# Kernel tuning notes

Hardware: AMD Instinct MI355X
Metric: run time of the kernel (lower is better)

## Reference

```python
import jax, jax.numpy as jnp
import numpy as np

B, T, D, U = 64, 2048, 256, 256
EPS = 1e-6


def setup_inputs() -> dict:
    key = jax.random.key(0)
    ks = jax.random.split(key, 4)
    x = jax.random.normal(ks[0], (B, T, D), dtype=jnp.float32)
    # glorot-ish scaled init for stability
    kernel = jax.random.normal(ks[1], (D, 3 * U), dtype=jnp.float32) * (1.0 / np.sqrt(D))
    rec_kernel = jax.random.normal(ks[2], (U, 3 * U), dtype=jnp.float32) * (1.0 / np.sqrt(U))
    bias = jnp.zeros((3 * U,), dtype=jnp.float32)
    ln_gamma = jnp.ones((U,), dtype=jnp.float32)
    ln_beta = jnp.zeros((U,), dtype=jnp.float32)
    return {"x": x, "kernel": kernel, "rec_kernel": rec_kernel, "bias": bias,
            "ln_gamma": ln_gamma, "ln_beta": ln_beta}


def _custom_gru(x, kernel, rec_kernel, bias):
    # Precompute input projection for all timesteps: [B,T,3U]
    xw = jnp.einsum('btd,dk->btk', x, kernel) + bias
    xw_t = jnp.swapaxes(xw, 0, 1)  # [T,B,3U] for scan
    h0 = jnp.zeros((x.shape[0], U), dtype=x.dtype)

    def step(h, xw_step):
        gates = xw_step + h @ rec_kernel            # [B,3U]
        z, r, h_hat_pre = jnp.split(gates, 3, axis=1)
        z = jax.nn.sigmoid(z)
        r = jax.nn.sigmoid(r)
        # nonstandard blend inside tanh (faithful to CustomGRUCell)
        h_hat = jnp.tanh(r * h_hat_pre + (1.0 - r) * h)
        h_new = (1.0 - z) * h_hat + z * h
        return h_new, h_new

    _, hs = jax.lax.scan(step, h0, xw_t)            # hs: [T,B,U]
    return jnp.swapaxes(hs, 0, 1)                   # [B,T,U]


def _layernorm(x, gamma, beta):
    mu = jnp.mean(x, axis=-1, keepdims=True)
    var = jnp.mean(jnp.square(x - mu), axis=-1, keepdims=True)
    return (x - mu) * jax.lax.rsqrt(var + EPS) * gamma + beta


def reference(x, kernel, rec_kernel, bias, ln_gamma, ln_beta):
    # call() returns only the GRU-stack branch (n=1 layer) + shared LayerNorm;
    # the embedded_inputs branch in the source is dead code.
    seq = _custom_gru(x, kernel, rec_kernel, bias)
    return _layernorm(seq, ln_gamma, ln_beta)
```

## Files before the change

### kernel.cpp

```cpp
#include <hip/hip_runtime.h>
#include <hip/hip_bf16.h>
#include <hip/hip_fp16.h>

using half2_t = __attribute__((ext_vector_type(2))) _Float16;
using half8_t = __attribute__((ext_vector_type(8))) _Float16;
using f32x4   = __attribute__((ext_vector_type(4))) float;
using i32x4   = __attribute__((ext_vector_type(4))) int;

#define B_   64
#define T_   2048
#define D_   256
#define U_   256
#define NG   768
#define TC   512
#define NCHUNK (T_/TC)
#define GB_SCAN 16
#define GB_GEMM 1536
#define GB_LN   2048

typedef const __attribute__((address_space(1))) void* gptr_t;
typedef __attribute__((address_space(3))) void* lptr_t;

__device__ __forceinline__ float rcpf(float x) { return __builtin_amdgcn_rcpf(x); }


__global__ void conv_x_chunk(const float* __restrict__ x, _Float16* __restrict__ xh, int t0) {
  size_t idx = ((size_t)blockIdx.x * 256 + threadIdx.x) * 8;
  int b   = (int)(idx >> 17);
  int rem = (int)(idx & 131071);
  const float4* p = (const float4*)(x + ((size_t)(b * T_ + t0)) * D_ + rem);
  float4 v0 = p[0], v1 = p[1];
  half8_t o;
  o[0] = (_Float16)v0.x; o[1] = (_Float16)v0.y; o[2] = (_Float16)v0.z; o[3] = (_Float16)v0.w;
  o[4] = (_Float16)v1.x; o[5] = (_Float16)v1.y; o[6] = (_Float16)v1.z; o[7] = (_Float16)v1.w;
  *(half8_t*)(xh + idx) = o;
}

__global__ void conv_T(const float* __restrict__ src, _Float16* __restrict__ dst) {
  int idx = blockIdx.x * 256 + threadIdx.x;
  int d = idx / NG;
  int j = idx - d * NG;
  dst[j * 256 + d] = (_Float16)src[idx];
}

__global__ void init_scale(unsigned* s) { if (threadIdx.x == 0) *s = 0u; }

__global__ void absmax_rec(const float* __restrict__ rec, unsigned* __restrict__ s) {
  int i = (blockIdx.x * 256 + threadIdx.x) * 4;
  float4 v = *(const float4*)(rec + i);
  float m = fmaxf(fmaxf(fabsf(v.x), fabsf(v.y)), fmaxf(fabsf(v.z), fabsf(v.w)));
  #pragma unroll
  for (int off = 32; off >= 1; off >>= 1) m = fmaxf(m, __shfl_xor(m, off));
  __shared__ float sm[4];
  int l = threadIdx.x & 63, wv = threadIdx.x >> 6;
  if (l == 0) sm[wv] = m;
  __syncthreads();
  if (threadIdx.x == 0) {
    m = fmaxf(fmaxf(sm[0], sm[1]), fmaxf(sm[2], sm[3]));
    atomicMax(s, __float_as_uint(m));
  }
}

__global__ void conv_rec_i8(const float* __restrict__ rec, const unsigned* __restrict__ sc,
                            char* __restrict__ dst) {
  int idx = blockIdx.x * 256 + threadIdx.x;
  int j = idx & 15, l = (idx >> 4) & 63, sl = idx >> 10;
  int mt = sl >> 2, ks = sl & 3, bi = l & 15, hi = l >> 4;
  float am = __uint_as_float(*sc) + 1e-30f;
  float s = 127.f / am;
  float v = rec[(size_t)(ks * 64 + hi * 16 + j) * NG + mt * 16 + bi] * s;
  int q = __float2int_rn(v);
  q = q > 127 ? 127 : (q < -127 ? -127 : q);
  dst[idx] = (char)q;
}


__global__ __launch_bounds__(1024) void mega(
    const char* __restrict__ rq,
    const _Float16* __restrict__ xwsS,
    const unsigned* __restrict__ sc,
    float* __restrict__ out,
    float* __restrict__ hg,
    int scanT0,
    const _Float16* __restrict__ xhc,
    const _Float16* __restrict__ kT,
    const float* __restrict__ bias,
    _Float16* __restrict__ xwsG,
    const float* __restrict__ gamma,
    const float* __restrict__ beta,
    int lnT0,
    int nScan, int nGemm)
{
  __shared__ union UU {
    struct { char Hq[2][1024]; } s;
    struct { alignas(16) _Float16 As[128 * 32]; alignas(16) _Float16 Bs[128 * 32]; } g;
  } U;

  int bid = blockIdx.x;
  const int tid = threadIdx.x;

  if (bid < nScan) {
    const int g = bid;
    const int w = tid >> 6, l = tid & 63, bi = l & 15, hi = l >> 4;
    const int bc = bi & 3, qq = bi >> 2;
    const int u = w * 16 + hi * 4 + qq;

    const i32x4* rp = (const i32x4*)rq;
#define FR(mt, ks) rp[((mt) * 4 + (ks)) * 64 + l]
    i32x4 Az0 = FR(w, 0),      Az1 = FR(w, 1),      Az2 = FR(w, 2),      Az3 = FR(w, 3);
    i32x4 Ar0 = FR(16 + w, 0), Ar1 = FR(16 + w, 1), Ar2 = FR(16 + w, 2), Ar3 = FR(16 + w, 3);
    i32x4 Ah0 = FR(32 + w, 0), Ah1 = FR(32 + w, 1), Ah2 = FR(32 + w, 2), Ah3 = FR(32 + w, 3);
#undef FR
    asm volatile("" : "+v"(Az0), "+v"(Az1), "+v"(Az2), "+v"(Az3),
                      "+v"(Ar0), "+v"(Ar1), "+v"(Ar2), "+v"(Ar3),
                      "+v"(Ah0), "+v"(Ah1), "+v"(Ah2), "+v"(Ah3));

    const float dq = (__uint_as_float(*sc) + 1e-30f) / (127.f * 127.f);

    float h = (scanT0 == 0) ? 0.f : hg[(size_t)(g * 4 + bc) * 256 + u];

    const int hwa = bc * 256 + ((w ^ bc) << 4) + hi * 4 + qq;
    { int q8 = __float2int_rn(h * 127.f); U.s.Hq[0][hwa] = (char)q8; }

    const char* xpg = (const char*)xwsS + (size_t)g * TC * 6144;
    float* outp = out + ((size_t)(g * 4 + bc) * T_ + scanT0) * U_ + u;

    unsigned nzr = *(const unsigned*)(xpg + tid * 4);
    _Float16 nh2 = *(const _Float16*)(xpg + 4096 + tid * 2);
    __syncthreads();

    for (int t = 0; t < TC; ++t) {
      half2_t zrp = __builtin_bit_cast(half2_t, nzr);
      float xzf = (float)zrp[0], xrf = (float)zrp[1], xhf = (float)nh2;
      {
        int tn = (t + 1 < TC) ? (t + 1) : t;
        nzr = *(const unsigned*)(xpg + (size_t)tn * 6144 + tid * 4);
        nh2 = *(const _Float16*)(xpg + (size_t)tn * 6144 + 4096 + tid * 2);
      }

      const char* hb = &U.s.Hq[t & 1][0];
      i32x4 az = {}, ar = {}, ah = {};
#define BADDR(ks) (bc * 256 + ((((ks) * 4 + hi) ^ bc) << 4))
      { i32x4 Bf;
        Bf = *(const i32x4*)(hb + BADDR(0));
        az = __builtin_amdgcn_mfma_i32_16x16x64_i8(Az0, Bf, az, 0, 0, 0);
        ar = __builtin_amdgcn_mfma_i32_16x16x64_i8(Ar0, Bf, ar, 0, 0, 0);
        ah = __builtin_amdgcn_mfma_i32_16x16x64_i8(Ah0, Bf, ah, 0, 0, 0);
        Bf = *(const i32x4*)(hb + BADDR(1));
        az = __builtin_amdgcn_mfma_i32_16x16x64_i8(Az1, Bf, az, 0, 0, 0);
        ar = __builtin_amdgcn_mfma_i32_16x16x64_i8(Ar1, Bf, ar, 0, 0, 0);
        ah = __builtin_amdgcn_mfma_i32_16x16x64_i8(Ah1, Bf, ah, 0, 0, 0);
        Bf = *(const i32x4*)(hb + BADDR(2));
        az = __builtin_amdgcn_mfma_i32_16x16x64_i8(Az2, Bf, az, 0, 0, 0);
        ar = __builtin_amdgcn_mfma_i32_16x16x64_i8(Ar2, Bf, ar, 0, 0, 0);
        ah = __builtin_amdgcn_mfma_i32_16x16x64_i8(Ah2, Bf, ah, 0, 0, 0);
        Bf = *(const i32x4*)(hb + BADDR(3));
        az = __builtin_amdgcn_mfma_i32_16x16x64_i8(Az3, Bf, az, 0, 0, 0);
        ar = __builtin_amdgcn_mfma_i32_16x16x64_i8(Ar3, Bf, ar, 0, 0, 0);
        ah = __builtin_amdgcn_mfma_i32_16x16x64_i8(Ah3, Bf, ah, 0, 0, 0);
      }
#undef BADDR

#define SEL4(a) ((qq & 2) ? ((qq & 1) ? (a)[3] : (a)[2]) : ((qq & 1) ? (a)[1] : (a)[0]))
      float pz = (float)SEL4(az) * dq + xzf;
      float pr = (float)SEL4(ar) * dq + xrf;
      float ph = (float)SEL4(ah) * dq + xhf;
#undef SEL4
      float z  = rcpf(1.f + __expf(-pz));
      float r  = rcpf(1.f + __expf(-pr));
      float y  = r * (ph - h) + h;
      float th = 2.f * rcpf(1.f + __expf(-2.f * y)) - 1.f;
      h = z * (h - th) + th;

      outp[(size_t)t * U_] = h;
      int q8 = __float2int_rn(h * 127.f);
      U.s.Hq[(t & 1) ^ 1][hwa] = (char)q8;
      __syncthreads();
    }

    hg[(size_t)(g * 4 + bc) * 256 + u] = h;
    return;
  }
  bid -= nScan;

  if (bid < nGemm) {
    const int tile = bid;
    const int mt = tile / 6, nt = tile % 6;
    const int w = tid >> 6, l = tid & 63;
    const int wm = (w & 3) * 32, wn = (w >> 2) * 32;
    const char* Ab = (const char*)xhc + (size_t)mt * 128 * 512;
    const char* Bb = (const char*)kT  + (size_t)nt * 128 * 512;
    f32x4 acc[2][2] = {};

    const bool isA = tid < 512;
    const int cc = isA ? tid : tid - 512;
    const int srow = cc >> 2, sgq = cc & 3;
    const int sgs = sgq ^ ((srow >> 1) & 3);
    const char* sb = isA ? Ab : Bb;
    char* ldsb = (char*)(isA ? U.g.As : U.g.Bs) + cc * 16;

    for (int kt = 0; kt < 8; ++kt) {
      __builtin_amdgcn_global_load_lds(
        (gptr_t)(sb + (size_t)srow * 512 + kt * 64 + sgs * 16),
        (lptr_t)ldsb, 16, 0, 0);
      __syncthreads();

      half8_t av[2], bv[2];
      #pragma unroll
      for (int mi = 0; mi < 2; ++mi) {
        int row = wm + mi * 16 + (l & 15);
        int off = row * 64 + (((l >> 4) ^ ((row >> 1) & 3)) << 4);
        av[mi] = *(const half8_t*)((const char*)U.g.As + off);
      }
      #pragma unroll
      for (int ni = 0; ni < 2; ++ni) {
        int row = wn + ni * 16 + (l & 15);
        int off = row * 64 + (((l >> 4) ^ ((row >> 1) & 3)) << 4);
        bv[ni] = *(const half8_t*)((const char*)U.g.Bs + off);
      }
      #pragma unroll
      for (int mi = 0; mi < 2; ++mi)
        #pragma unroll
        for (int ni = 0; ni < 2; ++ni)
          acc[mi][ni] = __builtin_amdgcn_mfma_f32_16x16x32_f16(av[mi], bv[ni], acc[mi][ni], 0, 0, 0);
      __syncthreads();
    }

    #pragma unroll
    for (int mi = 0; mi < 2; ++mi) {
      #pragma unroll
      for (int ni = 0; ni < 2; ++ni) {
        int c = nt * 128 + wn + ni * 16 + (l & 15);
        int cgate = c >> 8, uu = c & 255;
        int wv = uu >> 4, hq = (uu >> 2) & 3, qv = uu & 3;
        int lane_tid = wv * 64 + (qv << 2) + (hq << 4);
        float bc = bias[c];
        #pragma unroll
        for (int q = 0; q < 4; ++q) {
          int arow = mt * 128 + wm + mi * 16 + ((l >> 4) * 4 + q);
          int b = arow >> 9, tloc = arow & 511;
          int g = b >> 2, bidx = b & 3;
          int lane = lane_tid + bidx;
          size_t page = (size_t)(g * 512 + tloc) * 3072;
          size_t dst = (cgate < 2) ? (page + (size_t)lane * 2 + cgate)
                                   : (page + 2048 + lane);
          xwsG[dst] = (_Float16)(acc[mi][ni][q] + bc);
        }
      }
    }
    return;
  }
  bid -= nGemm;

  {
    int rid = bid * 16 + (tid >> 6);
    int l = tid & 63;
    int b = rid >> 9, tl = rid & 511;
    float* p = out + ((size_t)b * T_ + lnT0 + tl) * U_ + l * 4;
    f32x4 v = *(const f32x4*)p;
    float s  = (v[0] + v[1]) + (v[2] + v[3]);
    float s2 = (v[0]*v[0] + v[1]*v[1]) + (v[2]*v[2] + v[3]*v[3]);
    #pragma unroll
    for (int off = 1; off <= 32; off <<= 1) {
      s  += __shfl_xor(s, off);
      s2 += __shfl_xor(s2, off);
    }
    float mu = s * (1.f / 256.f);
    float var = s2 * (1.f / 256.f) - mu * mu;
    float rs = rsqrtf(var + 1e-6f);
    f32x4 gm = *(const f32x4*)(gamma + l * 4);
    f32x4 bt = *(const f32x4*)(beta + l * 4);
    f32x4 o;
    o[0] = (v[0] - mu) * rs * gm[0] + bt[0];
    o[1] = (v[1] - mu) * rs * gm[1] + bt[1];
    o[2] = (v[2] - mu) * rs * gm[2] + bt[2];
    o[3] = (v[3] - mu) * rs * gm[3] + bt[3];
    *(f32x4*)p = o;
  }
}

extern "C" void kernel_launch(void* const* d_in, const int* in_sizes, int n_in,
                              void* d_out, int out_size, void* d_ws, size_t ws_size,
                              hipStream_t stream) {
  const float* x     = (const float*)d_in[0];
  const float* kern  = (const float*)d_in[1];
  const float* rec   = (const float*)d_in[2];
  const float* bias  = (const float*)d_in[3];
  const float* gamma = (const float*)d_in[4];
  const float* beta  = (const float*)d_in[5];
  float* out = (float*)d_out;
  char* ws = (char*)d_ws;

  const size_t XWS = 50331648;
  const bool pipe = (ws_size >= 118096000ull);

  _Float16* xwsA = (_Float16*)ws;
  _Float16* xwsB = pipe ? (_Float16*)(ws + XWS) : xwsA;
  size_t o = pipe ? 2 * XWS : XWS;
  _Float16* xhc = (_Float16*)(ws + o);           o += 16777216;
  _Float16* kT  = (_Float16*)(ws + o);           o += 393216;
  char*     rq  = (char*)    (ws + o);           o += 196608;
  unsigned* sc  = (unsigned*)(ws + o);           o += 128;
  float*    hg  = (float*)   (ws + o);

  init_scale<<<1, 64, 0, stream>>>(sc);
  absmax_rec<<<192, 256, 0, stream>>>(rec, sc);
  conv_T<<<768, 256, 0, stream>>>(kern, kT);
  conv_rec_i8<<<768, 256, 0, stream>>>(rec, sc, rq);

  if (pipe) {
    _Float16* xb[2] = { xwsA, xwsB };
    conv_x_chunk<<<4096, 256, 0, stream>>>(x, xhc, 0);
    mega<<<GB_GEMM, 1024, 0, stream>>>(rq, xwsA, sc, out, hg, 0,
                                       xhc, kT, bias, xwsA, gamma, beta, 0,
                                       0, GB_GEMM);
    conv_x_chunk<<<4096, 256, 0, stream>>>(x, xhc, TC);
    mega<<<GB_SCAN + GB_GEMM, 1024, 0, stream>>>(rq, xwsA, sc, out, hg, 0,
                                       xhc, kT, bias, xwsB, gamma, beta, 0,
                                       GB_SCAN, GB_GEMM);
    conv_x_chunk<<<4096, 256, 0, stream>>>(x, xhc, 2 * TC);
    mega<<<GB_SCAN + GB_GEMM + GB_LN, 1024, 0, stream>>>(rq, xwsB, sc, out, hg, TC,
                                       xhc, kT, bias, xwsA, gamma, beta, 0,
                                       GB_SCAN, GB_GEMM);
    conv_x_chunk<<<4096, 256, 0, stream>>>(x, xhc, 3 * TC);
    mega<<<GB_SCAN + GB_GEMM + GB_LN, 1024, 0, stream>>>(rq, xwsA, sc, out, hg, 2 * TC,
                                       xhc, kT, bias, xwsB, gamma, beta, TC,
                                       GB_SCAN, GB_GEMM);
    mega<<<GB_SCAN + GB_LN, 1024, 0, stream>>>(rq, xwsB, sc, out, hg, 3 * TC,
                                       xhc, kT, bias, xwsA, gamma, beta, 2 * TC,
                                       GB_SCAN, 0);
    mega<<<GB_LN, 1024, 0, stream>>>(rq, xwsA, sc, out, hg, 0,
                                       xhc, kT, bias, xwsA, gamma, beta, 3 * TC,
                                       0, 0);
    (void)xb;
  } else {
    for (int c = 0; c < NCHUNK; ++c) {
      int t0 = c * TC;
      conv_x_chunk<<<4096, 256, 0, stream>>>(x, xhc, t0);
      mega<<<GB_GEMM, 1024, 0, stream>>>(rq, xwsA, sc, out, hg, t0,
                                         xhc, kT, bias, xwsA, gamma, beta, t0,
                                         0, GB_GEMM);
      mega<<<GB_SCAN, 1024, 0, stream>>>(rq, xwsA, sc, out, hg, t0,
                                         xhc, kT, bias, xwsA, gamma, beta, t0,
                                         GB_SCAN, 0);
      mega<<<GB_LN, 1024, 0, stream>>>(rq, xwsA, sc, out, hg, t0,
                                       xhc, kT, bias, xwsA, gamma, beta, t0,
                                       0, 0);
    }
  }
}
```

Before: 1.466 ms.

## Split scan across 32 workgroups with 2 batches each, 8 active waves

The recurrent scan now uses 32 workgroups, each handling 2 batch rows instead of 4. Only 8 waves per workgroup compute, and each wave holds twice as many int8 weight fragments, pinned in AGPRs. The idle waves just match the barrier count. The GEMM epilogue's scattered output layout is changed to fit the new per-thread mapping. The goal is to shorten the serial per-step critical path and spread the recurrence over more CUs, at the cost of more MFMAs per wave and more register pressure.

```diff
diff --git a/kernel.cpp b/kernel.cpp
--- a/kernel.cpp
+++ b/kernel.cpp
@@ -14,7 +14,7 @@
 #define NG   768
 #define TC   512
 #define NCHUNK (T_/TC)
-#define GB_SCAN 16
+#define GB_SCAN 32
 #define GB_GEMM 1536
 #define GB_LN   2048
 
@@ -92,7 +92,7 @@
     int nScan, int nGemm)
 {
   __shared__ union UU {
-    struct { char Hq[2][1024]; } s;
+    struct { alignas(16) char Hq[2][512]; } s;
     struct { alignas(16) _Float16 As[128 * 32]; alignas(16) _Float16 Bs[128 * 32]; } g;
   } U;
 
@@ -102,83 +102,106 @@
   if (bid < nScan) {
     const int g = bid;
     const int w = tid >> 6, l = tid & 63, bi = l & 15, hi = l >> 4;
-    const int bc = bi & 3, qq = bi >> 2;
-    const int u = w * 16 + hi * 4 + qq;
-
-    const i32x4* rp = (const i32x4*)rq;
+    if (w < 8) {
+      const int bc = bi & 1;
+      const int sq = bi >> 1;
+      const int s2 = sq >> 2, qq = sq & 3;
+      const int u = 32 * w + s2 * 16 + hi * 4 + qq;
+
+      const i32x4* rp = (const i32x4*)rq;
 #define FR(mt, ks) rp[((mt) * 4 + (ks)) * 64 + l]
-    i32x4 Az0 = FR(w, 0),      Az1 = FR(w, 1),      Az2 = FR(w, 2),      Az3 = FR(w, 3);
-    i32x4 Ar0 = FR(16 + w, 0), Ar1 = FR(16 + w, 1), Ar2 = FR(16 + w, 2), Ar3 = FR(16 + w, 3);
-    i32x4 Ah0 = FR(32 + w, 0), Ah1 = FR(32 + w, 1), Ah2 = FR(32 + w, 2), Ah3 = FR(32 + w, 3);
+      i32x4 Z00 = FR(2*w, 0),    Z01 = FR(2*w, 1),    Z02 = FR(2*w, 2),    Z03 = FR(2*w, 3);
+      i32x4 Z10 = FR(2*w+1, 0),  Z11 = FR(2*w+1, 1),  Z12 = FR(2*w+1, 2),  Z13 = FR(2*w+1, 3);
+      i32x4 R00 = FR(16+2*w, 0), R01 = FR(16+2*w, 1), R02 = FR(16+2*w, 2), R03 = FR(16+2*w, 3);
+      i32x4 R10 = FR(17+2*w, 0), R11 = FR(17+2*w, 1), R12 = FR(17+2*w, 2), R13 = FR(17+2*w, 3);
+      i32x4 H00 = FR(32+2*w, 0), H01 = FR(32+2*w, 1), H02 = FR(32+2*w, 2), H03 = FR(32+2*w, 3);
+      i32x4 H10 = FR(33+2*w, 0), H11 = FR(33+2*w, 1), H12 = FR(33+2*w, 2), H13 = FR(33+2*w, 3);
 #undef FR
-    asm volatile("" : "+v"(Az0), "+v"(Az1), "+v"(Az2), "+v"(Az3),
-                      "+v"(Ar0), "+v"(Ar1), "+v"(Ar2), "+v"(Ar3),
-                      "+v"(Ah0), "+v"(Ah1), "+v"(Ah2), "+v"(Ah3));
-
-    const float dq = (__uint_as_float(*sc) + 1e-30f) / (127.f * 127.f);
-
-    float h = (scanT0 == 0) ? 0.f : hg[(size_t)(g * 4 + bc) * 256 + u];
-
-    const int hwa = bc * 256 + ((w ^ bc) << 4) + hi * 4 + qq;
-    { int q8 = __float2int_rn(h * 127.f); U.s.Hq[0][hwa] = (char)q8; }
-
-    const char* xpg = (const char*)xwsS + (size_t)g * TC * 6144;
-    float* outp = out + ((size_t)(g * 4 + bc) * T_ + scanT0) * U_ + u;
-
-    unsigned nzr = *(const unsigned*)(xpg + tid * 4);
-    _Float16 nh2 = *(const _Float16*)(xpg + 4096 + tid * 2);
-    __syncthreads();
-
-    for (int t = 0; t < TC; ++t) {
-      half2_t zrp = __builtin_bit_cast(half2_t, nzr);
-      float xzf = (float)zrp[0], xrf = (float)zrp[1], xhf = (float)nh2;
-      {
-        int tn = (t + 1 < TC) ? (t + 1) : t;
-        nzr = *(const unsigned*)(xpg + (size_t)tn * 6144 + tid * 4);
-        nh2 = *(const _Float16*)(xpg + (size_t)tn * 6144 + 4096 + tid * 2);
+      asm volatile("" : "+a"(Z00), "+a"(Z01), "+a"(Z02), "+a"(Z03),
+                        "+a"(Z10), "+a"(Z11), "+a"(Z12), "+a"(Z13));
+      asm volatile("" : "+a"(R00), "+a"(R01), "+a"(R02), "+a"(R03),
+                        "+a"(R10), "+a"(R11), "+a"(R12), "+a"(R13));
+      asm volatile("" : "+a"(H00), "+a"(H01), "+a"(H02), "+a"(H03),
+                        "+a"(H10), "+a"(H11), "+a"(H12), "+a"(H13));
+
+      const float dq = (__uint_as_float(*sc) + 1e-30f) / (127.f * 127.f);
+
+      float h = (scanT0 == 0) ? 0.f : hg[(size_t)(g * 2 + bc) * 256 + u];
+
+      const int hwa = bc * 256 + u;
+      { int q8 = __float2int_rn(h * 127.f); U.s.Hq[0][hwa] = (char)q8; }
+
+      const char* xpg = (const char*)xwsS + (size_t)g * TC * 3072;
+      float* outp = out + ((size_t)(g * 2 + bc) * T_ + scanT0) * U_ + u;
+
+      unsigned nzr = *(const unsigned*)(xpg + tid * 4);
+      _Float16 nh2 = *(const _Float16*)(xpg + 2048 + tid * 2);
+      __syncthreads();
+
+      for (int t = 0; t < TC; ++t) {
+        half2_t zrp = __builtin_bit_cast(half2_t, nzr);
+        float xzf = (float)zrp[0], xrf = (float)zrp[1], xhf = (float)nh2;
+        {
+          int tn = (t + 1 < TC) ? (t + 1) : t;
+          nzr = *(const unsigned*)(xpg + (size_t)tn * 3072 + tid * 4);
+          nh2 = *(const _Float16*)(xpg + (size_t)tn * 3072 + 2048 + tid * 2);
+        }
+
+        const char* hb = &U.s.Hq[t & 1][0];
+        i32x4 az0 = {}, az1 = {}, ar0 = {}, ar1 = {}, ah0 = {}, ah1 = {};
+        { i32x4 Bf;
+          Bf = *(const i32x4*)(hb + bc * 256 + 0 * 64 + hi * 16);
+          az0 = __builtin_amdgcn_mfma_i32_16x16x64_i8(Z00, Bf, az0, 0, 0, 0);
+          az1 = __builtin_amdgcn_mfma_i32_16x16x64_i8(Z10, Bf, az1, 0, 0, 0);
+          ar0 = __builtin_amdgcn_mfma_i32_16x16x64_i8(R00, Bf, ar0, 0, 0, 0);
+          ar1 = __builtin_amdgcn_mfma_i32_16x16x64_i8(R10, Bf, ar1, 0, 0, 0);
+          ah0 = __builtin_amdgcn_mfma_i32_16x16x64_i8(H00, Bf, ah0, 0, 0, 0);
+          ah1 = __builtin_amdgcn_mfma_i32_16x16x64_i8(H10, Bf, ah1, 0, 0, 0);
+          Bf = *(const i32x4*)(hb + bc * 256 + 1 * 64 + hi * 16);
+          az0 = __builtin_amdgcn_mfma_i32_16x16x64_i8(Z01, Bf, az0, 0, 0, 0);
+          az1 = __builtin_amdgcn_mfma_i32_16x16x64_i8(Z11, Bf, az1, 0, 0, 0);
+          ar0 = __builtin_amdgcn_mfma_i32_16x16x64_i8(R01, Bf, ar0, 0, 0, 0);
+          ar1 = __builtin_amdgcn_mfma_i32_16x16x64_i8(R11, Bf, ar1, 0, 0, 0);
+          ah0 = __builtin_amdgcn_mfma_i32_16x16x64_i8(H01, Bf, ah0, 0, 0, 0);
+          ah1 = __builtin_amdgcn_mfma_i32_16x16x64_i8(H11, Bf, ah1, 0, 0, 0);
+          Bf = *(const i32x4*)(hb + bc * 256 + 2 * 64 + hi * 16);
+          az0 = __builtin_amdgcn_mfma_i32_16x16x64_i8(Z02, Bf, az0, 0, 0, 0);
+          az1 = __builtin_amdgcn_mfma_i32_16x16x64_i8(Z12, Bf, az1, 0, 0, 0);
+          ar0 = __builtin_amdgcn_mfma_i32_16x16x64_i8(R02, Bf, ar0, 0, 0, 0);
+          ar1 = __builtin_amdgcn_mfma_i32_16x16x64_i8(R12, Bf, ar1, 0, 0, 0);
+          ah0 = __builtin_amdgcn_mfma_i32_16x16x64_i8(H02, Bf, ah0, 0, 0, 0);
+          ah1 = __builtin_amdgcn_mfma_i32_16x16x64_i8(H12, Bf, ah1, 0, 0, 0);
+          Bf = *(const i32x4*)(hb + bc * 256 + 3 * 64 + hi * 16);
+          az0 = __builtin_amdgcn_mfma_i32_16x16x64_i8(Z03, Bf, az0, 0, 0, 0);
+          az1 = __builtin_amdgcn_mfma_i32_16x16x64_i8(Z13, Bf, az1, 0, 0, 0);
+          ar0 = __builtin_amdgcn_mfma_i32_16x16x64_i8(R03, Bf, ar0, 0, 0, 0);
+          ar1 = __builtin_amdgcn_mfma_i32_16x16x64_i8(R13, Bf, ar1, 0, 0, 0);
+          ah0 = __builtin_amdgcn_mfma_i32_16x16x64_i8(H03, Bf, ah0, 0, 0, 0);
+          ah1 = __builtin_amdgcn_mfma_i32_16x16x64_i8(H13, Bf, ah1, 0, 0, 0);
+        }
+
+#define SEL4(a) ((qq & 2) ? ((qq & 1) ? (a)[3] : (a)[2]) : ((qq & 1) ? (a)[1] : (a)[0]))
+        int azi = s2 ? SEL4(az1) : SEL4(az0);
+        int ari = s2 ? SEL4(ar1) : SEL4(ar0);
+        int ahi = s2 ? SEL4(ah1) : SEL4(ah0);
+#undef SEL4
+        float z  = rcpf(1.f + __expf(-fmaf((float)azi, dq, xzf)));
+        float r  = rcpf(1.f + __expf(-fmaf((float)ari, dq, xrf)));
+        float ph = fmaf((float)ahi, dq, xhf);
+        float y  = fmaf(r, ph - h, h);
+        float th = fmaf(2.f, rcpf(1.f + __expf(-2.f * y)), -1.f);
+        h = fmaf(z, h - th, th);
+
+        outp[(size_t)t * U_] = h;
+        int q8 = __float2int_rn(h * 127.f);
+        U.s.Hq[(t & 1) ^ 1][hwa] = (char)q8;
+        __syncthreads();
       }
 
-      const char* hb = &U.s.Hq[t & 1][0];
-      i32x4 az = {}, ar = {}, ah = {};
-#define BADDR(ks) (bc * 256 + ((((ks) * 4 + hi) ^ bc) << 4))
-      { i32x4 Bf;
-        Bf = *(const i32x4*)(hb + BADDR(0));
-        az = __builtin_amdgcn_mfma_i32_16x16x64_i8(Az0, Bf, az, 0, 0, 0);
-        ar = __builtin_amdgcn_mfma_i32_16x16x64_i8(Ar0, Bf, ar, 0, 0, 0);
-        ah = __builtin_amdgcn_mfma_i32_16x16x64_i8(Ah0, Bf, ah, 0, 0, 0);
-        Bf = *(const i32x4*)(hb + BADDR(1));
-        az = __builtin_amdgcn_mfma_i32_16x16x64_i8(Az1, Bf, az, 0, 0, 0);
-        ar = __builtin_amdgcn_mfma_i32_16x16x64_i8(Ar1, Bf, ar, 0, 0, 0);
-        ah = __builtin_amdgcn_mfma_i32_16x16x64_i8(Ah1, Bf, ah, 0, 0, 0);
-        Bf = *(const i32x4*)(hb + BADDR(2));
-        az = __builtin_amdgcn_mfma_i32_16x16x64_i8(Az2, Bf, az, 0, 0, 0);
-        ar = __builtin_amdgcn_mfma_i32_16x16x64_i8(Ar2, Bf, ar, 0, 0, 0);
-        ah = __builtin_amdgcn_mfma_i32_16x16x64_i8(Ah2, Bf, ah, 0, 0, 0);
-        Bf = *(const i32x4*)(hb + BADDR(3));
-        az = __builtin_amdgcn_mfma_i32_16x16x64_i8(Az3, Bf, az, 0, 0, 0);
-        ar = __builtin_amdgcn_mfma_i32_16x16x64_i8(Ar3, Bf, ar, 0, 0, 0);
-        ah = __builtin_amdgcn_mfma_i32_16x16x64_i8(Ah3, Bf, ah, 0, 0, 0);
-      }
-#undef BADDR
-
-#define SEL4(a) ((qq & 2) ? ((qq & 1) ? (a)[3] : (a)[2]) : ((qq & 1) ? (a)[1] : (a)[0]))
-      float pz = (float)SEL4(az) * dq + xzf;
-      float pr = (float)SEL4(ar) * dq + xrf;
-      float ph = (float)SEL4(ah) * dq + xhf;
-#undef SEL4
-      float z  = rcpf(1.f + __expf(-pz));
-      float r  = rcpf(1.f + __expf(-pr));
-      float y  = r * (ph - h) + h;
-      float th = 2.f * rcpf(1.f + __expf(-2.f * y)) - 1.f;
-      h = z * (h - th) + th;
-
-      outp[(size_t)t * U_] = h;
-      int q8 = __float2int_rn(h * 127.f);
-      U.s.Hq[(t & 1) ^ 1][hwa] = (char)q8;
-      __syncthreads();
-    }
-
-    hg[(size_t)(g * 4 + bc) * 256 + u] = h;
+      hg[(size_t)(g * 2 + bc) * 256 + u] = h;
+    } else {
+      for (int t = 0; t <= TC; ++t) __syncthreads();
+    }
     return;
   }
   bid -= nScan;
@@ -231,19 +254,19 @@
       #pragma unroll
       for (int ni = 0; ni < 2; ++ni) {
         int c = nt * 128 + wn + ni * 16 + (l & 15);
-        int cgate = c >> 8, uu = c & 255;
-        int wv = uu >> 4, hq = (uu >> 2) & 3, qv = uu & 3;
-        int lane_tid = wv * 64 + (qv << 2) + (hq << 4);
+        int cgate = c >> 8, u2 = c & 255;
+        int wv = u2 >> 5, s2 = (u2 >> 4) & 1, hi2 = (u2 >> 2) & 3, q2 = u2 & 3;
+        int stidBase = wv * 64 + hi2 * 16 + (((s2 << 2) | q2) << 1);
         float bc = bias[c];
         #pragma unroll
         for (int q = 0; q < 4; ++q) {
           int arow = mt * 128 + wm + mi * 16 + ((l >> 4) * 4 + q);
           int b = arow >> 9, tloc = arow & 511;
-          int g = b >> 2, bidx = b & 3;
-          int lane = lane_tid + bidx;
-          size_t page = (size_t)(g * 512 + tloc) * 3072;
-          size_t dst = (cgate < 2) ? (page + (size_t)lane * 2 + cgate)
-                                   : (page + 2048 + lane);
+          int gg = b >> 1, bcl = b & 1;
+          int stid = stidBase + bcl;
+          size_t pageH = (size_t)(gg * 512 + tloc) * 1536;
+          size_t dst = (cgate < 2) ? (pageH + (size_t)stid * 2 + cgate)
+                                   : (pageH + 1024 + stid);
           xwsG[dst] = (_Float16)(acc[mi][ni][q] + bc);
         }
       }
@@ -309,7 +332,6 @@
   conv_rec_i8<<<768, 256, 0, stream>>>(rec, sc, rq);
 
   if (pipe) {
-    _Float16* xb[2] = { xwsA, xwsB };
     conv_x_chunk<<<4096, 256, 0, stream>>>(x, xhc, 0);
     mega<<<GB_GEMM, 1024, 0, stream>>>(rq, xwsA, sc, out, hg, 0,
                                        xhc, kT, bias, xwsA, gamma, beta, 0,
@@ -332,7 +354,6 @@
     mega<<<GB_LN, 1024, 0, stream>>>(rq, xwsA, sc, out, hg, 0,
                                        xhc, kT, bias, xwsA, gamma, beta, 3 * TC,
                                        0, 0);
-    (void)xb;
   } else {
     for (int c = 0; c < NCHUNK; ++c) {
       int t0 = c * TC;
```

Result: slower. 4.557 ms (+210.8%).
